# Kernel optimization log

Measured on AMD Instinct MI355X. Metric: run time of the kernel, lower is better.

The kernel has to match this reference:

```python
import jax, jax.numpy as jnp
import numpy as np

B = 8192      # batch
C = 4096      # in_channels
K = 5         # group_size (odd, centered window)


def setup_inputs() -> dict:
    key = jax.random.key(0)
    kx, kw, kb = jax.random.split(key, 3)
    x = jax.random.normal(kx, (B, C), dtype=jnp.float32)
    # Banded weights: W[i, k] multiplies x[:, i + k - K//2] (zero outside range).
    W = jax.random.normal(kw, (C, K), dtype=jnp.float32) * 0.1
    b = jax.random.normal(kb, (C,), dtype=jnp.float32) * 0.1
    return {"x": x, "W": W, "b": b}


def reference(x, W, b):
    # out[:, i] = sum_k W[i, k] * x[:, i + k - K//2] + b[i]
    # Boundary clipping in the original == zero padding here.
    Bn, Cn = x.shape
    Kn = W.shape[1]
    half = Kn // 2
    xp = jnp.pad(x, ((0, 0), (half, half)))  # [B, C + K - 1]
    acc = jnp.zeros_like(x)
    for k in range(Kn):  # tiny fixed loop (K=5), fused shift-multiply-add
        acc = acc + xp[:, k:k + Cn] * W[:, k]
    return acc + b
```

## Files before the change

kernel.cpp:

```cpp
#include <hip/hip_runtime.h>


#define B_ROWS 8192
#define C_CH   4096
#define KWIN   5
#define ROWS_PER_BLOCK 16

__global__ __launch_bounds__(256) void grouped_linear_kernel(
    const float* __restrict__ x, const float* __restrict__ W,
    const float* __restrict__ bias, float* __restrict__ out)
{
    const int chunk = (blockIdx.x << 8) + threadIdx.x;
    const int c     = chunk << 2;
    const int r0    = blockIdx.y * ROWS_PER_BLOCK;

    const float4* W4 = (const float4*)(W + (size_t)c * KWIN);
    const float4 w0 = W4[0];
    const float4 w1 = W4[1];
    const float4 w2 = W4[2];
    const float4 w3 = W4[3];
    const float4 w4 = W4[4];
    const float4 bv = ((const float4*)bias)[chunk];

    const bool has_m = (c > 0);
    const bool has_p = (c + 4 < C_CH);
    const float4 zero = make_float4(0.f, 0.f, 0.f, 0.f);

    const float4* xrow = (const float4*)(x   + (size_t)r0 * C_CH);
    float4*       orow = (float4*)      (out + (size_t)r0 * C_CH);

    #pragma unroll 2
    for (int r = 0; r < ROWS_PER_BLOCK; ++r) {
        const float4 xm = has_m ? xrow[chunk - 1] : zero;
        const float4 xc = xrow[chunk];
        const float4 xp = has_p ? xrow[chunk + 1] : zero;

        const float win0 = xm.z, win1 = xm.w;
        const float win2 = xc.x, win3 = xc.y, win4 = xc.z, win5 = xc.w;
        const float win6 = xp.x, win7 = xp.y;

        float4 o;
        o.x = fmaf(w0.x, win0, fmaf(w0.y, win1, fmaf(w0.z, win2, fmaf(w0.w, win3, fmaf(w1.x, win4, bv.x)))));
        o.y = fmaf(w1.y, win1, fmaf(w1.z, win2, fmaf(w1.w, win3, fmaf(w2.x, win4, fmaf(w2.y, win5, bv.y)))));
        o.z = fmaf(w2.z, win2, fmaf(w2.w, win3, fmaf(w3.x, win4, fmaf(w3.y, win5, fmaf(w3.z, win6, bv.z)))));
        o.w = fmaf(w3.w, win3, fmaf(w4.x, win4, fmaf(w4.y, win5, fmaf(w4.z, win6, fmaf(w4.w, win7, bv.w)))));

        orow[chunk] = o;
        xrow += C_CH / 4;
        orow += C_CH / 4;
    }
}

extern "C" void kernel_launch(void* const* d_in, const int* in_sizes, int n_in,
                              void* d_out, int out_size, void* d_ws, size_t ws_size,
                              hipStream_t stream) {
    const float* x    = (const float*)d_in[0];
    const float* W    = (const float*)d_in[1];
    const float* bias = (const float*)d_in[2];
    float* out = (float*)d_out;

    dim3 grid(C_CH / 4 / 256, B_ROWS / ROWS_PER_BLOCK);
    dim3 block(256);
    grouped_linear_kernel<<<grid, block, 0, stream>>>(x, W, bias, out);
}
```

Measured before the change: 250.6 us.

## Batch row loads ahead of compute and use nontemporal output stores

Rows per block drop from 16 to 8, and each thread now issues the loads for 4 rows at once before computing, which gives more memory-level parallelism per thread. Outputs are written with nontemporal stores so the streamed output does not pollute the cache. The grid doubles in height and more live registers are needed per thread.

```diff
diff --git a/kernel.cpp b/kernel.cpp
--- a/kernel.cpp
+++ b/kernel.cpp
@@ -4,7 +4,10 @@
 #define B_ROWS 8192
 #define C_CH   4096
 #define KWIN   5
-#define ROWS_PER_BLOCK 16
+#define ROWS_PER_BLOCK 8
+#define RBATCH 4
+
+typedef float nfloat4 __attribute__((ext_vector_type(4)));
 
 __global__ __launch_bounds__(256) void grouped_linear_kernel(
     const float* __restrict__ x, const float* __restrict__ W,
@@ -27,27 +30,37 @@
     const float4 zero = make_float4(0.f, 0.f, 0.f, 0.f);
 
     const float4* xrow = (const float4*)(x   + (size_t)r0 * C_CH);
-    float4*       orow = (float4*)      (out + (size_t)r0 * C_CH);
+    nfloat4*      orow = (nfloat4*)     (out + (size_t)r0 * C_CH);
+    const int row_stride = C_CH / 4;
 
-    #pragma unroll 2
-    for (int r = 0; r < ROWS_PER_BLOCK; ++r) {
-        const float4 xm = has_m ? xrow[chunk - 1] : zero;
-        const float4 xc = xrow[chunk];
-        const float4 xp = has_p ? xrow[chunk + 1] : zero;
+    for (int rb = 0; rb < ROWS_PER_BLOCK; rb += RBATCH) {
+        float4 xm[RBATCH], xc[RBATCH], xp[RBATCH];
 
-        const float win0 = xm.z, win1 = xm.w;
-        const float win2 = xc.x, win3 = xc.y, win4 = xc.z, win5 = xc.w;
-        const float win6 = xp.x, win7 = xp.y;
+        #pragma unroll
+        for (int i = 0; i < RBATCH; ++i) {
+            const float4* xr = xrow + (size_t)i * row_stride;
+            xm[i] = has_m ? xr[chunk - 1] : zero;
+            xc[i] = xr[chunk];
+            xp[i] = has_p ? xr[chunk + 1] : zero;
+        }
 
-        float4 o;
-        o.x = fmaf(w0.x, win0, fmaf(w0.y, win1, fmaf(w0.z, win2, fmaf(w0.w, win3, fmaf(w1.x, win4, bv.x)))));
-        o.y = fmaf(w1.y, win1, fmaf(w1.z, win2, fmaf(w1.w, win3, fmaf(w2.x, win4, fmaf(w2.y, win5, bv.y)))));
-        o.z = fmaf(w2.z, win2, fmaf(w2.w, win3, fmaf(w3.x, win4, fmaf(w3.y, win5, fmaf(w3.z, win6, bv.z)))));
-        o.w = fmaf(w3.w, win3, fmaf(w4.x, win4, fmaf(w4.y, win5, fmaf(w4.z, win6, fmaf(w4.w, win7, bv.w)))));
+        #pragma unroll
+        for (int i = 0; i < RBATCH; ++i) {
+            const float win0 = xm[i].z, win1 = xm[i].w;
+            const float win2 = xc[i].x, win3 = xc[i].y, win4 = xc[i].z, win5 = xc[i].w;
+            const float win6 = xp[i].x, win7 = xp[i].y;
 
-        orow[chunk] = o;
-        xrow += C_CH / 4;
-        orow += C_CH / 4;
+            nfloat4 o;
+            o.x = fmaf(w0.x, win0, fmaf(w0.y, win1, fmaf(w0.z, win2, fmaf(w0.w, win3, fmaf(w1.x, win4, bv.x)))));
+            o.y = fmaf(w1.y, win1, fmaf(w1.z, win2, fmaf(w1.w, win3, fmaf(w2.x, win4, fmaf(w2.y, win5, bv.y)))));
+            o.z = fmaf(w2.z, win2, fmaf(w2.w, win3, fmaf(w3.x, win4, fmaf(w3.y, win5, fmaf(w3.z, win6, bv.z)))));
+            o.w = fmaf(w3.w, win3, fmaf(w4.x, win4, fmaf(w4.y, win5, fmaf(w4.z, win6, fmaf(w4.w, win7, bv.w)))));
+
+            __builtin_nontemporal_store(o, orow + (size_t)i * row_stride + chunk);
+        }
+
+        xrow += (size_t)RBATCH * row_stride;
+        orow += (size_t)RBATCH * row_stride;
     }
 }
 
```

Result: slower. 258.2 us (+3.0%).
